# Kernel tuning notes

Measured on AMD Instinct MI355X. Metric: run time of the kernel, lower is better.

The kernel has to match this reference:

```python
import jax, jax.numpy as jnp
import numpy as np

N_USERS = 200000
N_ITEMS = 100000
EMBED_DIM = 64
N_LAYERS = 3
N_INTER = 1000000


def setup_inputs() -> dict:
    key = jax.random.key(0)
    k1, k2, k3, k4 = jax.random.split(key, 4)
    user_ids = jax.random.randint(k1, (N_INTER,), 0, N_USERS, dtype=jnp.int64 if jax.config.jax_enable_x64 else jnp.int32)
    item_ids = jax.random.randint(k2, (N_INTER,), 0, N_ITEMS, dtype=jnp.int64 if jax.config.jax_enable_x64 else jnp.int32)
    user_emb = jax.random.normal(k3, (N_USERS, EMBED_DIM), dtype=jnp.float32) * 0.1
    item_emb = jax.random.normal(k4, (N_ITEMS, EMBED_DIM), dtype=jnp.float32) * 0.1
    return {"user_emb": user_emb, "item_emb": item_emb, "user_ids": user_ids, "item_ids": item_ids}


def reference(user_emb, item_emb, user_ids, item_ids):
    n_users = user_emb.shape[0]
    n_items = item_emb.shape[0]
    n_nodes = n_users + n_items

    # Symmetric bipartite adjacency as directed edge list (both directions).
    src = jnp.concatenate([user_ids, item_ids + n_users])   # [2E]
    dst = jnp.concatenate([item_ids + n_users, user_ids])   # [2E]

    # Symmetric normalization D^{-1/2} A D^{-1/2} (duplicate edges sum, matching scipy CSR).
    deg = jax.ops.segment_sum(jnp.ones_like(src, dtype=jnp.float32), src, num_segments=n_nodes)
    d_inv_sqrt = jnp.where(deg > 0, jax.lax.rsqrt(jnp.maximum(deg, 1.0)), 0.0)
    w = d_inv_sqrt[src] * d_inv_sqrt[dst]                    # [2E] edge weights

    emb = jnp.concatenate([user_emb, item_emb], axis=0)      # [n_nodes, d]
    acc = emb
    for _ in range(N_LAYERS):
        # SpMM: out[dst] += w * emb[src]
        emb = jax.ops.segment_sum(w[:, None] * emb[src], dst, num_segments=n_nodes)
        acc = acc + emb
    final = acc / (N_LAYERS + 1)                             # mean over stacked layers
    return final[:n_users], final[n_users:]
```

## Files before the change

### kernel.cpp

```cpp
#include <hip/hip_runtime.h>

#define N_USERS 200000
#define N_ITEMS 100000
#define N_NODES 300000
#define DIM 64
#define N_INTER 1000000
#define N_EDGES (2 * N_INTER)

#define BSHIFT 10
#define BNODES (1 << BSHIFT)
#define NBUCKET ((N_NODES + BNODES - 1) >> BSHIFT)
#define TILE 4096
#define NBLK_P ((N_INTER + TILE - 1) / TILE)

#define NPW 8
#define NWAVE ((N_NODES + NPW - 1) / NPW)
#define GATHER_THREADS (NWAVE * 64)

typedef unsigned short bf16_t;
typedef unsigned int u32;

static __device__ __forceinline__ bf16_t f2bf(float f) {
    union { float f; u32 u; } v; v.f = f;
    u32 r = v.u + 0x7FFFu + ((v.u >> 16) & 1u);
    return (bf16_t)(r >> 16);
}
static __device__ __forceinline__ float bf2f(bf16_t h) {
    union { u32 u; float f; } v; v.u = ((u32)h) << 16;
    return v.f;
}
static __device__ __forceinline__ float bflo(u32 v) {
    union { u32 u; float f; } x; x.u = v << 16; return x.f;
}
static __device__ __forceinline__ float bfhi(u32 v) {
    union { u32 u; float f; } x; x.u = v & 0xFFFF0000u; return x.f;
}
static __device__ __forceinline__ u32 pack_bf16(float lo, float hi) {
    u32 r;
    asm("v_cvt_pk_bf16_f32 %0, %1, %2" : "=v"(r) : "v"(lo), "v"(hi));
    return r;
}

__global__ void hist_kernel(const int* __restrict__ uid, const int* __restrict__ iid,
                            u32* __restrict__ bucket_count) {
    __shared__ u32 h[NBUCKET];
    int t = threadIdx.x;
    for (int i = t; i < NBUCKET; i += 256) h[i] = 0;
    __syncthreads();
    int base = blockIdx.x * TILE;
    int end = base + TILE; if (end > N_INTER) end = N_INTER;
    for (int k = base + t; k < end; k += 256) {
        int u = uid[k];
        int it = N_USERS + iid[k];
        atomicAdd(&h[it >> BSHIFT], 1u);
        atomicAdd(&h[u >> BSHIFT], 1u);
    }
    __syncthreads();
    for (int i = t; i < NBUCKET; i += 256)
        if (h[i]) atomicAdd(&bucket_count[i], h[i]);
}

__global__ void scan_kernel(const u32* __restrict__ bucket_count, u32* __restrict__ bstart,
                            u32* __restrict__ bucket_cursor, u32* __restrict__ rowptr) {
    __shared__ u32 buf[2][512];
    int t = threadIdx.x;
    u32 v0 = (t < NBUCKET) ? bucket_count[t] : 0u;
    buf[0][t] = v0;
    __syncthreads();
    int s = 0;
    for (int off = 1; off < 512; off <<= 1) {
        u32 v = buf[s][t];
        if (t >= off) v += buf[s][t - off];
        buf[1 - s][t] = v;
        __syncthreads();
        s = 1 - s;
    }
    if (t < NBUCKET) {
        u32 excl = buf[s][t] - v0;
        bstart[t] = excl;
        bucket_cursor[t] = excl;
    }
    if (t == 0) {
        bstart[NBUCKET] = N_EDGES;
        rowptr[N_NODES] = N_EDGES;
    }
}

__global__ void place_kernel(const int* __restrict__ uid, const int* __restrict__ iid,
                             u32* __restrict__ bucket_cursor, u32* __restrict__ bdata) {
    __shared__ u32 h[NBUCKET];
    __shared__ u32 basesh[NBUCKET];
    int t = threadIdx.x;
    for (int i = t; i < NBUCKET; i += 256) h[i] = 0;
    __syncthreads();
    int base = blockIdx.x * TILE;
    int end = base + TILE; if (end > N_INTER) end = N_INTER;
    for (int k = base + t; k < end; k += 256) {
        int u = uid[k];
        int it = N_USERS + iid[k];
        atomicAdd(&h[it >> BSHIFT], 1u);
        atomicAdd(&h[u >> BSHIFT], 1u);
    }
    __syncthreads();
    for (int i = t; i < NBUCKET; i += 256) {
        u32 c = h[i];
        basesh[i] = c ? atomicAdd(&bucket_cursor[i], c) : 0u;
        h[i] = 0;
    }
    __syncthreads();
    for (int k = base + t; k < end; k += 256) {
        int u = uid[k];
        int it = N_USERS + iid[k];
        {
            int b = it >> BSHIFT;
            u32 pos = basesh[b] + atomicAdd(&h[b], 1u);
            bdata[pos] = (((u32)(it & (BNODES - 1))) << 19) | (u32)u;
        }
        {
            int b = u >> BSHIFT;
            u32 pos = basesh[b] + atomicAdd(&h[b], 1u);
            bdata[pos] = (((u32)(u & (BNODES - 1))) << 19) | (u32)it;
        }
    }
}

__global__ void csr_kernel(const u32* __restrict__ bstart, const u32* __restrict__ bdata,
                           u32* __restrict__ rowptr, float* __restrict__ dinv,
                           int* __restrict__ col) {
    __shared__ u32 cnt[BNODES];
    __shared__ u32 sb[2][BNODES];
    __shared__ u32 cur[BNODES];
    int b = blockIdx.x;
    int t = threadIdx.x;
    int nbase = b << BSHIFT;
    u32 bs = bstart[b], be = bstart[b + 1];
    u32 m = be - bs;

    #pragma unroll
    for (int j = 0; j < 4; ++j) cnt[t + j * 256] = 0;
    __syncthreads();
    for (u32 e = t; e < m; e += 256) {
        u32 v = bdata[bs + e];
        atomicAdd(&cnt[v >> 19], 1u);
    }
    __syncthreads();
    #pragma unroll
    for (int j = 0; j < 4; ++j) sb[0][t + j * 256] = cnt[t + j * 256];
    __syncthreads();
    int s = 0;
    for (int off = 1; off < BNODES; off <<= 1) {
        #pragma unroll
        for (int j = 0; j < 4; ++j) {
            int idx = t + j * 256;
            u32 v = sb[s][idx];
            if (idx >= off) v += sb[s][idx - off];
            sb[1 - s][idx] = v;
        }
        __syncthreads();
        s = 1 - s;
    }
    #pragma unroll
    for (int j = 0; j < 4; ++j) {
        int idx = t + j * 256;
        int node = nbase + idx;
        u32 c = cnt[idx];
        u32 excl = sb[s][idx] - c;
        cur[idx] = excl;
        if (node < N_NODES) {
            rowptr[node] = bs + excl;
            dinv[node] = (c > 0) ? rsqrtf((float)c) : 0.0f;
        }
    }
    __syncthreads();
    for (u32 e = t; e < m; e += 256) {
        u32 v = bdata[bs + e];
        u32 ln = v >> 19;
        u32 pos = atomicAdd(&cur[ln], 1u);
        col[bs + pos] = (int)(v & 0x7FFFFu);
    }
}

__global__ void ecol_kernel(const int* __restrict__ col, const float* __restrict__ dinv,
                            int2* __restrict__ ecol) {
    int e = blockIdx.x * blockDim.x + threadIdx.x;
    if (e < N_EDGES) {
        int s = col[e];
        ecol[e] = make_int2(s, __float_as_int(dinv[s]));
    }
}

__global__ void init_kernel(const float4* __restrict__ ue, const float4* __restrict__ ie,
                            ushort4* __restrict__ cur) {
    int idx = blockIdx.x * blockDim.x + threadIdx.x;
    if (idx < N_NODES * 16) {
        float4 v = (idx < N_USERS * 16) ? ue[idx] : ie[idx - N_USERS * 16];
        ushort4 h;
        h.x = f2bf(v.x); h.y = f2bf(v.y); h.z = f2bf(v.z); h.w = f2bf(v.w);
        cur[idx] = h;
    }
}

__global__ void gather_kernel(const u32* __restrict__ rowptr, const int2* __restrict__ ecol,
                              const float* __restrict__ dinv,
                              const u32* __restrict__ cur, u32* __restrict__ nxt) {
    int wid = (blockIdx.x * blockDim.x + threadIdx.x) >> 6;
    int lane = threadIdx.x & 63;
    int n0 = __builtin_amdgcn_readfirstlane(wid * NPW);
    if (n0 >= N_NODES) return;
    u32 rp[NPW + 1];
    #pragma unroll
    for (int i = 0; i <= NPW; ++i) rp[i] = rowptr[n0 + i];
    bool hi = (lane >> 5) != 0;
    u32 c = (u32)(lane & 31);
    #pragma unroll
    for (int pr = 0; pr < NPW; pr += 2) {
        u32 rsA = rp[pr],     lA = rp[pr + 1] - rp[pr];
        u32 rsB = rp[pr + 1], lB = rp[pr + 2] - rp[pr + 1];
        u32 mx = lA > lB ? lA : lB;
        float a0 = 0.0f, a1 = 0.0f;
        for (u32 p = 0; p < mx; p += 4) {
            #pragma unroll
            for (int q = 0; q < 4; ++q) {
                u32 st = p + (u32)q;
                u32 iA = rsA + st; if (iA >= (u32)N_EDGES) iA = N_EDGES - 1u;
                u32 iB = rsB + st; if (iB >= (u32)N_EDGES) iB = N_EDGES - 1u;
                iA = __builtin_amdgcn_readfirstlane((int)iA);
                iB = __builtin_amdgcn_readfirstlane((int)iB);
                int2 eA = ecol[iA];
                int2 eB = ecol[iB];
                u32 wAu = (st < lA) ? (u32)eA.y : 0u;
                u32 wBu = (st < lB) ? (u32)eB.y : 0u;
                u32 srow = hi ? (u32)eB.x : (u32)eA.x;
                float wf = __uint_as_float(hi ? wBu : wAu);
                u32 v = cur[(srow << 5) + c];
                a0 += wf * bflo(v);
                a1 += wf * bfhi(v);
            }
        }
        float sc = hi ? dinv[n0 + pr + 1] : dinv[n0 + pr];
        u32 orow = (((u32)(n0 + pr) + (hi ? 1u : 0u)) << 5) + c;
        nxt[orow] = pack_bf16(sc * a0, sc * a1);
    }
}

__global__ void gather_final_kernel(const u32* __restrict__ rowptr, const int2* __restrict__ ecol,
                                    const float* __restrict__ dinv,
                                    const u32* __restrict__ b1, const u32* __restrict__ b2,
                                    const float* __restrict__ ue, const float* __restrict__ ie,
                                    float* __restrict__ out) {
    int wid = (blockIdx.x * blockDim.x + threadIdx.x) >> 6;
    int lane = threadIdx.x & 63;
    int n0 = __builtin_amdgcn_readfirstlane(wid * NPW);
    if (n0 >= N_NODES) return;
    u32 rp[NPW + 1];
    #pragma unroll
    for (int i = 0; i <= NPW; ++i) rp[i] = rowptr[n0 + i];
    bool hi = (lane >> 5) != 0;
    u32 c = (u32)(lane & 31);
    #pragma unroll
    for (int pr = 0; pr < NPW; pr += 2) {
        u32 rsA = rp[pr],     lA = rp[pr + 1] - rp[pr];
        u32 rsB = rp[pr + 1], lB = rp[pr + 2] - rp[pr + 1];
        u32 mx = lA > lB ? lA : lB;
        float a0 = 0.0f, a1 = 0.0f;
        for (u32 p = 0; p < mx; p += 4) {
            #pragma unroll
            for (int q = 0; q < 4; ++q) {
                u32 st = p + (u32)q;
                u32 iA = rsA + st; if (iA >= (u32)N_EDGES) iA = N_EDGES - 1u;
                u32 iB = rsB + st; if (iB >= (u32)N_EDGES) iB = N_EDGES - 1u;
                iA = __builtin_amdgcn_readfirstlane((int)iA);
                iB = __builtin_amdgcn_readfirstlane((int)iB);
                int2 eA = ecol[iA];
                int2 eB = ecol[iB];
                u32 wAu = (st < lA) ? (u32)eA.y : 0u;
                u32 wBu = (st < lB) ? (u32)eB.y : 0u;
                u32 srow = hi ? (u32)eB.x : (u32)eA.x;
                float wf = __uint_as_float(hi ? wBu : wAu);
                u32 v = b2[(srow << 5) + c];
                a0 += wf * bflo(v);
                a1 += wf * bfhi(v);
            }
        }
        int n = n0 + pr + (hi ? 1 : 0);
        float sc = hi ? dinv[n0 + pr + 1] : dinv[n0 + pr];
        u32 o32 = (((u32)n) << 5) + c;
        u32 v1 = b1[o32], v2 = b2[o32];
        float2 e0 = (n < N_USERS) ? ((const float2*)ue)[o32]
                                  : ((const float2*)ie)[o32 - (u32)N_USERS * 32u];
        float ox = (e0.x + bflo(v1) + bflo(v2) + sc * a0) * 0.25f;
        float oy = (e0.y + bfhi(v1) + bfhi(v2) + sc * a1) * 0.25f;
        ((float2*)out)[o32] = make_float2(ox, oy);
    }
}

extern "C" void kernel_launch(void* const* d_in, const int* in_sizes, int n_in,
                              void* d_out, int out_size, void* d_ws, size_t ws_size,
                              hipStream_t stream) {
    const float* ue = (const float*)d_in[0];
    const float* ie = (const float*)d_in[1];
    const int* uid = (const int*)d_in[2];
    const int* iid = (const int*)d_in[3];
    float* out = (float*)d_out;

    char* ws = (char*)d_ws;
    size_t off = 0;
    auto alloc = [&](size_t bytes) { char* p = ws + off; off = (off + bytes + 255) & ~(size_t)255; return p; };
    u32*    bucket_count  = (u32*)alloc((size_t)NBUCKET * 4);
    u32*    bstart        = (u32*)alloc((size_t)(NBUCKET + 1) * 4);
    u32*    bucket_cursor = (u32*)alloc((size_t)NBUCKET * 4);
    u32*    rowptr        = (u32*)alloc((size_t)(N_NODES + 1) * 4);
    float*  dinv          = (float*)alloc((size_t)N_NODES * 4);
    u32*    bdata         = (u32*)alloc((size_t)N_EDGES * 4);
    int*    col           = (int*)alloc((size_t)N_EDGES * 4);
    int2*   ecol          = (int2*)alloc((size_t)N_EDGES * 8);
    bf16_t* buf0          = (bf16_t*)alloc((size_t)N_NODES * DIM * 2);
    bf16_t* buf1          = (bf16_t*)alloc((size_t)N_NODES * DIM * 2);
    bf16_t* buf2          = (bf16_t*)alloc((size_t)N_NODES * DIM * 2);

    hipMemsetAsync(bucket_count, 0, (size_t)NBUCKET * 4, stream);
    hist_kernel<<<NBLK_P, 256, 0, stream>>>(uid, iid, bucket_count);
    scan_kernel<<<1, 512, 0, stream>>>(bucket_count, bstart, bucket_cursor, rowptr);
    place_kernel<<<NBLK_P, 256, 0, stream>>>(uid, iid, bucket_cursor, bdata);
    csr_kernel<<<NBUCKET, 256, 0, stream>>>(bstart, bdata, rowptr, dinv, col);
    ecol_kernel<<<(N_EDGES + 255) / 256, 256, 0, stream>>>(col, dinv, ecol);

    init_kernel<<<(N_NODES * 16 + 255) / 256, 256, 0, stream>>>(
        (const float4*)ue, (const float4*)ie, (ushort4*)buf0);

    gather_kernel<<<(GATHER_THREADS + 255) / 256, 256, 0, stream>>>(
        rowptr, ecol, dinv, (const u32*)buf0, (u32*)buf1);
    gather_kernel<<<(GATHER_THREADS + 255) / 256, 256, 0, stream>>>(
        rowptr, ecol, dinv, (const u32*)buf1, (u32*)buf2);
    gather_final_kernel<<<(GATHER_THREADS + 255) / 256, 256, 0, stream>>>(
        rowptr, ecol, dinv, (const u32*)buf1, (const u32*)buf2, ue, ie, out);
}
```

Before: 424.2 us.

## Store per-block bucket histograms and compute placement offsets with a per-bucket scan

The hist kernel now writes each tile's bucket histogram to a workspace array. A new base_kernel scans those histograms across blocks for each bucket to produce exact write offsets. This lets place_kernel skip recounting its tile and skip the global atomic cursor reservation. Bucket size and tile size are also halved, which doubles the number of csr_kernel blocks and shrinks its shared-memory scan. In exchange the pipeline gains an extra launch and a strided read/write of the per-block histogram matrix.

```diff
diff --git a/kernel.cpp b/kernel.cpp
--- a/kernel.cpp
+++ b/kernel.cpp
@@ -7,10 +7,10 @@
 #define N_INTER 1000000
 #define N_EDGES (2 * N_INTER)
 
-#define BSHIFT 10
+#define BSHIFT 9
 #define BNODES (1 << BSHIFT)
 #define NBUCKET ((N_NODES + BNODES - 1) >> BSHIFT)
-#define TILE 4096
+#define TILE 2048
 #define NBLK_P ((N_INTER + TILE - 1) / TILE)
 
 #define NPW 8
@@ -42,7 +42,7 @@
 }
 
 __global__ void hist_kernel(const int* __restrict__ uid, const int* __restrict__ iid,
-                            u32* __restrict__ bucket_count) {
+                            u32* __restrict__ bucket_count, u32* __restrict__ bhist) {
     __shared__ u32 h[NBUCKET];
     int t = threadIdx.x;
     for (int i = t; i < NBUCKET; i += 256) h[i] = 0;
@@ -56,15 +56,41 @@
         atomicAdd(&h[u >> BSHIFT], 1u);
     }
     __syncthreads();
-    for (int i = t; i < NBUCKET; i += 256)
-        if (h[i]) atomicAdd(&bucket_count[i], h[i]);
+    u32* bh = bhist + (size_t)blockIdx.x * NBUCKET;
+    for (int i = t; i < NBUCKET; i += 256) {
+        u32 c = h[i];
+        bh[i] = c;
+        if (c) atomicAdd(&bucket_count[i], c);
+    }
 }
 
 __global__ void scan_kernel(const u32* __restrict__ bucket_count, u32* __restrict__ bstart,
-                            u32* __restrict__ bucket_cursor, u32* __restrict__ rowptr) {
+                            u32* __restrict__ rowptr) {
+    __shared__ u32 buf[2][1024];
+    int t = threadIdx.x;
+    u32 v0 = (t < NBUCKET) ? bucket_count[t] : 0u;
+    buf[0][t] = v0;
+    __syncthreads();
+    int s = 0;
+    for (int off = 1; off < 1024; off <<= 1) {
+        u32 v = buf[s][t];
+        if (t >= off) v += buf[s][t - off];
+        buf[1 - s][t] = v;
+        __syncthreads();
+        s = 1 - s;
+    }
+    if (t < NBUCKET) bstart[t] = buf[s][t] - v0;
+    if (t == 0) {
+        bstart[NBUCKET] = N_EDGES;
+        rowptr[N_NODES] = N_EDGES;
+    }
+}
+
+__global__ void base_kernel(const u32* __restrict__ bstart, u32* __restrict__ bhist) {
     __shared__ u32 buf[2][512];
-    int t = threadIdx.x;
-    u32 v0 = (t < NBUCKET) ? bucket_count[t] : 0u;
+    int bkt = blockIdx.x;
+    int t = threadIdx.x;
+    u32 v0 = (t < NBLK_P) ? bhist[(size_t)t * NBUCKET + bkt] : 0u;
     buf[0][t] = v0;
     __syncthreads();
     int s = 0;
@@ -75,39 +101,23 @@
         __syncthreads();
         s = 1 - s;
     }
-    if (t < NBUCKET) {
-        u32 excl = buf[s][t] - v0;
-        bstart[t] = excl;
-        bucket_cursor[t] = excl;
-    }
-    if (t == 0) {
-        bstart[NBUCKET] = N_EDGES;
-        rowptr[N_NODES] = N_EDGES;
-    }
+    if (t < NBLK_P)
+        bhist[(size_t)t * NBUCKET + bkt] = bstart[bkt] + (buf[s][t] - v0);
 }
 
 __global__ void place_kernel(const int* __restrict__ uid, const int* __restrict__ iid,
-                             u32* __restrict__ bucket_cursor, u32* __restrict__ bdata) {
+                             const u32* __restrict__ bhist, u32* __restrict__ bdata) {
     __shared__ u32 h[NBUCKET];
     __shared__ u32 basesh[NBUCKET];
     int t = threadIdx.x;
-    for (int i = t; i < NBUCKET; i += 256) h[i] = 0;
+    const u32* bh = bhist + (size_t)blockIdx.x * NBUCKET;
+    for (int i = t; i < NBUCKET; i += 256) {
+        basesh[i] = bh[i];
+        h[i] = 0;
+    }
     __syncthreads();
     int base = blockIdx.x * TILE;
     int end = base + TILE; if (end > N_INTER) end = N_INTER;
-    for (int k = base + t; k < end; k += 256) {
-        int u = uid[k];
-        int it = N_USERS + iid[k];
-        atomicAdd(&h[it >> BSHIFT], 1u);
-        atomicAdd(&h[u >> BSHIFT], 1u);
-    }
-    __syncthreads();
-    for (int i = t; i < NBUCKET; i += 256) {
-        u32 c = h[i];
-        basesh[i] = c ? atomicAdd(&bucket_cursor[i], c) : 0u;
-        h[i] = 0;
-    }
-    __syncthreads();
     for (int k = base + t; k < end; k += 256) {
         int u = uid[k];
         int it = N_USERS + iid[k];
@@ -137,7 +147,7 @@
     u32 m = be - bs;
 
     #pragma unroll
-    for (int j = 0; j < 4; ++j) cnt[t + j * 256] = 0;
+    for (int j = 0; j < BNODES / 256; ++j) cnt[t + j * 256] = 0;
     __syncthreads();
     for (u32 e = t; e < m; e += 256) {
         u32 v = bdata[bs + e];
@@ -145,12 +155,12 @@
     }
     __syncthreads();
     #pragma unroll
-    for (int j = 0; j < 4; ++j) sb[0][t + j * 256] = cnt[t + j * 256];
+    for (int j = 0; j < BNODES / 256; ++j) sb[0][t + j * 256] = cnt[t + j * 256];
     __syncthreads();
     int s = 0;
     for (int off = 1; off < BNODES; off <<= 1) {
         #pragma unroll
-        for (int j = 0; j < 4; ++j) {
+        for (int j = 0; j < BNODES / 256; ++j) {
             int idx = t + j * 256;
             u32 v = sb[s][idx];
             if (idx >= off) v += sb[s][idx - off];
@@ -160,7 +170,7 @@
         s = 1 - s;
     }
     #pragma unroll
-    for (int j = 0; j < 4; ++j) {
+    for (int j = 0; j < BNODES / 256; ++j) {
         int idx = t + j * 256;
         int node = nbase + idx;
         u32 c = cnt[idx];
@@ -308,7 +318,7 @@
     auto alloc = [&](size_t bytes) { char* p = ws + off; off = (off + bytes + 255) & ~(size_t)255; return p; };
     u32*    bucket_count  = (u32*)alloc((size_t)NBUCKET * 4);
     u32*    bstart        = (u32*)alloc((size_t)(NBUCKET + 1) * 4);
-    u32*    bucket_cursor = (u32*)alloc((size_t)NBUCKET * 4);
+    u32*    bhist         = (u32*)alloc((size_t)NBLK_P * NBUCKET * 4);
     u32*    rowptr        = (u32*)alloc((size_t)(N_NODES + 1) * 4);
     float*  dinv          = (float*)alloc((size_t)N_NODES * 4);
     u32*    bdata         = (u32*)alloc((size_t)N_EDGES * 4);
@@ -319,9 +329,10 @@
     bf16_t* buf2          = (bf16_t*)alloc((size_t)N_NODES * DIM * 2);
 
     hipMemsetAsync(bucket_count, 0, (size_t)NBUCKET * 4, stream);
-    hist_kernel<<<NBLK_P, 256, 0, stream>>>(uid, iid, bucket_count);
-    scan_kernel<<<1, 512, 0, stream>>>(bucket_count, bstart, bucket_cursor, rowptr);
-    place_kernel<<<NBLK_P, 256, 0, stream>>>(uid, iid, bucket_cursor, bdata);
+    hist_kernel<<<NBLK_P, 256, 0, stream>>>(uid, iid, bucket_count, bhist);
+    scan_kernel<<<1, 1024, 0, stream>>>(bucket_count, bstart, rowptr);
+    base_kernel<<<NBUCKET, 512, 0, stream>>>(bstart, bhist);
+    place_kernel<<<NBLK_P, 256, 0, stream>>>(uid, iid, bhist, bdata);
     csr_kernel<<<NBUCKET, 256, 0, stream>>>(bstart, bdata, rowptr, dinv, col);
     ecol_kernel<<<(N_EDGES + 255) / 256, 256, 0, stream>>>(col, dinv, ecol);
 
```

Result: no change. 423.7 us (-0.1%).

## Build CSR via global per-node degree atomics and direct edge placement

Applied to the files above, without the earlier changes.

Replaces the bucketed two-level CSR build (bucket histogram, bucket placement, per-bucket local sort, separate ecol pass) with a per-node global atomic degree count, a three-stage block scan for rowptr, and a place kernel that writes (neighbor, dinv) pairs straight into ecol using per-node atomic cursors. This removes the intermediate bdata and col arrays and two passes over the edges. In exchange it relies on global atomics scattered across 300K nodes, and edge order within a row becomes nondeterministic, which can change the bf16 accumulation order and makes gather reads of neighbors less ordered.

```diff
diff --git a/kernel.cpp b/kernel.cpp
--- a/kernel.cpp
+++ b/kernel.cpp
@@ -7,11 +7,8 @@
 #define N_INTER 1000000
 #define N_EDGES (2 * N_INTER)
 
-#define BSHIFT 10
-#define BNODES (1 << BSHIFT)
-#define NBUCKET ((N_NODES + BNODES - 1) >> BSHIFT)
-#define TILE 4096
-#define NBLK_P ((N_INTER + TILE - 1) / TILE)
+#define SBLK 1024
+#define NSB ((N_NODES + SBLK - 1) / SBLK)
 
 #define NPW 8
 #define NWAVE ((N_NODES + NPW - 1) / NPW)
@@ -25,10 +22,6 @@
     u32 r = v.u + 0x7FFFu + ((v.u >> 16) & 1u);
     return (bf16_t)(r >> 16);
 }
-static __device__ __forceinline__ float bf2f(bf16_t h) {
-    union { u32 u; float f; } v; v.u = ((u32)h) << 16;
-    return v.f;
-}
 static __device__ __forceinline__ float bflo(u32 v) {
     union { u32 u; float f; } x; x.u = v << 16; return x.f;
 }
@@ -41,30 +34,41 @@
     return r;
 }
 
-__global__ void hist_kernel(const int* __restrict__ uid, const int* __restrict__ iid,
-                            u32* __restrict__ bucket_count) {
-    __shared__ u32 h[NBUCKET];
-    int t = threadIdx.x;
-    for (int i = t; i < NBUCKET; i += 256) h[i] = 0;
-    __syncthreads();
-    int base = blockIdx.x * TILE;
-    int end = base + TILE; if (end > N_INTER) end = N_INTER;
-    for (int k = base + t; k < end; k += 256) {
+__global__ void deg_kernel(const int* __restrict__ uid, const int* __restrict__ iid,
+                           u32* __restrict__ deg) {
+    int k = blockIdx.x * blockDim.x + threadIdx.x;
+    if (k < N_INTER) {
         int u = uid[k];
         int it = N_USERS + iid[k];
-        atomicAdd(&h[it >> BSHIFT], 1u);
-        atomicAdd(&h[u >> BSHIFT], 1u);
-    }
+        atomicAdd(&deg[it], 1u);
+        atomicAdd(&deg[u], 1u);
+    }
+}
+
+__global__ void s1_kernel(const u32* __restrict__ deg, u32* __restrict__ bsum) {
+    __shared__ u32 red[256];
+    int b = blockIdx.x, t = threadIdx.x;
+    int base = b * SBLK;
+    u32 s = 0;
+    #pragma unroll
+    for (int j = 0; j < 4; ++j) {
+        int idx = base + t + j * 256;
+        if (idx < N_NODES) s += deg[idx];
+    }
+    red[t] = s;
     __syncthreads();
-    for (int i = t; i < NBUCKET; i += 256)
-        if (h[i]) atomicAdd(&bucket_count[i], h[i]);
-}
-
-__global__ void scan_kernel(const u32* __restrict__ bucket_count, u32* __restrict__ bstart,
-                            u32* __restrict__ bucket_cursor, u32* __restrict__ rowptr) {
+    for (int off = 128; off > 0; off >>= 1) {
+        if (t < off) red[t] += red[t + off];
+        __syncthreads();
+    }
+    if (t == 0) bsum[b] = red[0];
+}
+
+__global__ void s2_kernel(const u32* __restrict__ bsum, u32* __restrict__ bbase,
+                          u32* __restrict__ rowptr) {
     __shared__ u32 buf[2][512];
     int t = threadIdx.x;
-    u32 v0 = (t < NBUCKET) ? bucket_count[t] : 0u;
+    u32 v0 = (t < NSB) ? bsum[t] : 0u;
     buf[0][t] = v0;
     __syncthreads();
     int s = 0;
@@ -75,117 +79,64 @@
         __syncthreads();
         s = 1 - s;
     }
-    if (t < NBUCKET) {
-        u32 excl = buf[s][t] - v0;
-        bstart[t] = excl;
-        bucket_cursor[t] = excl;
-    }
-    if (t == 0) {
-        bstart[NBUCKET] = N_EDGES;
-        rowptr[N_NODES] = N_EDGES;
-    }
-}
-
-__global__ void place_kernel(const int* __restrict__ uid, const int* __restrict__ iid,
-                             u32* __restrict__ bucket_cursor, u32* __restrict__ bdata) {
-    __shared__ u32 h[NBUCKET];
-    __shared__ u32 basesh[NBUCKET];
-    int t = threadIdx.x;
-    for (int i = t; i < NBUCKET; i += 256) h[i] = 0;
-    __syncthreads();
-    int base = blockIdx.x * TILE;
-    int end = base + TILE; if (end > N_INTER) end = N_INTER;
-    for (int k = base + t; k < end; k += 256) {
-        int u = uid[k];
-        int it = N_USERS + iid[k];
-        atomicAdd(&h[it >> BSHIFT], 1u);
-        atomicAdd(&h[u >> BSHIFT], 1u);
-    }
-    __syncthreads();
-    for (int i = t; i < NBUCKET; i += 256) {
-        u32 c = h[i];
-        basesh[i] = c ? atomicAdd(&bucket_cursor[i], c) : 0u;
-        h[i] = 0;
-    }
-    __syncthreads();
-    for (int k = base + t; k < end; k += 256) {
-        int u = uid[k];
-        int it = N_USERS + iid[k];
-        {
-            int b = it >> BSHIFT;
-            u32 pos = basesh[b] + atomicAdd(&h[b], 1u);
-            bdata[pos] = (((u32)(it & (BNODES - 1))) << 19) | (u32)u;
-        }
-        {
-            int b = u >> BSHIFT;
-            u32 pos = basesh[b] + atomicAdd(&h[b], 1u);
-            bdata[pos] = (((u32)(u & (BNODES - 1))) << 19) | (u32)it;
-        }
-    }
-}
-
-__global__ void csr_kernel(const u32* __restrict__ bstart, const u32* __restrict__ bdata,
-                           u32* __restrict__ rowptr, float* __restrict__ dinv,
-                           int* __restrict__ col) {
-    __shared__ u32 cnt[BNODES];
-    __shared__ u32 sb[2][BNODES];
-    __shared__ u32 cur[BNODES];
-    int b = blockIdx.x;
-    int t = threadIdx.x;
-    int nbase = b << BSHIFT;
-    u32 bs = bstart[b], be = bstart[b + 1];
-    u32 m = be - bs;
-
-    #pragma unroll
-    for (int j = 0; j < 4; ++j) cnt[t + j * 256] = 0;
-    __syncthreads();
-    for (u32 e = t; e < m; e += 256) {
-        u32 v = bdata[bs + e];
-        atomicAdd(&cnt[v >> 19], 1u);
-    }
-    __syncthreads();
-    #pragma unroll
-    for (int j = 0; j < 4; ++j) sb[0][t + j * 256] = cnt[t + j * 256];
+    if (t < NSB) bbase[t] = buf[s][t] - v0;
+    if (t == 0) rowptr[N_NODES] = N_EDGES;
+}
+
+__global__ void s3_kernel(const u32* __restrict__ deg, const u32* __restrict__ bbase,
+                          u32* __restrict__ rowptr, u32* __restrict__ gcur,
+                          float* __restrict__ dinv) {
+    __shared__ u32 sb[2][SBLK];
+    int b = blockIdx.x, t = threadIdx.x;
+    int base = b * SBLK;
+    u32 v[4];
+    #pragma unroll
+    for (int j = 0; j < 4; ++j) {
+        int idx = t + j * 256;
+        int node = base + idx;
+        v[j] = (node < N_NODES) ? deg[node] : 0u;
+        sb[0][idx] = v[j];
+    }
     __syncthreads();
     int s = 0;
-    for (int off = 1; off < BNODES; off <<= 1) {
+    for (int off = 1; off < SBLK; off <<= 1) {
         #pragma unroll
         for (int j = 0; j < 4; ++j) {
             int idx = t + j * 256;
-            u32 v = sb[s][idx];
-            if (idx >= off) v += sb[s][idx - off];
-            sb[1 - s][idx] = v;
+            u32 x = sb[s][idx];
+            if (idx >= off) x += sb[s][idx - off];
+            sb[1 - s][idx] = x;
         }
         __syncthreads();
         s = 1 - s;
     }
+    u32 bb = bbase[b];
     #pragma unroll
     for (int j = 0; j < 4; ++j) {
         int idx = t + j * 256;
-        int node = nbase + idx;
-        u32 c = cnt[idx];
-        u32 excl = sb[s][idx] - c;
-        cur[idx] = excl;
+        int node = base + idx;
         if (node < N_NODES) {
-            rowptr[node] = bs + excl;
-            dinv[node] = (c > 0) ? rsqrtf((float)c) : 0.0f;
-        }
-    }
-    __syncthreads();
-    for (u32 e = t; e < m; e += 256) {
-        u32 v = bdata[bs + e];
-        u32 ln = v >> 19;
-        u32 pos = atomicAdd(&cur[ln], 1u);
-        col[bs + pos] = (int)(v & 0x7FFFFu);
-    }
-}
-
-__global__ void ecol_kernel(const int* __restrict__ col, const float* __restrict__ dinv,
-                            int2* __restrict__ ecol) {
-    int e = blockIdx.x * blockDim.x + threadIdx.x;
-    if (e < N_EDGES) {
-        int s = col[e];
-        ecol[e] = make_int2(s, __float_as_int(dinv[s]));
+            u32 rp = bb + (sb[s][idx] - v[j]);
+            rowptr[node] = rp;
+            gcur[node] = rp;
+            dinv[node] = v[j] ? rsqrtf((float)v[j]) : 0.0f;
+        }
+    }
+}
+
+__global__ void place_kernel(const int* __restrict__ uid, const int* __restrict__ iid,
+                             const float* __restrict__ dinv, u32* __restrict__ gcur,
+                             int2* __restrict__ ecol) {
+    int k = blockIdx.x * blockDim.x + threadIdx.x;
+    if (k < N_INTER) {
+        int u = uid[k];
+        int it = N_USERS + iid[k];
+        float du = dinv[u];
+        float di = dinv[it];
+        u32 p1 = atomicAdd(&gcur[it], 1u);
+        ecol[p1] = make_int2(u, __float_as_int(du));
+        u32 p2 = atomicAdd(&gcur[u], 1u);
+        ecol[p2] = make_int2(it, __float_as_int(di));
     }
 }
 
@@ -306,24 +257,23 @@
     char* ws = (char*)d_ws;
     size_t off = 0;
     auto alloc = [&](size_t bytes) { char* p = ws + off; off = (off + bytes + 255) & ~(size_t)255; return p; };
-    u32*    bucket_count  = (u32*)alloc((size_t)NBUCKET * 4);
-    u32*    bstart        = (u32*)alloc((size_t)(NBUCKET + 1) * 4);
-    u32*    bucket_cursor = (u32*)alloc((size_t)NBUCKET * 4);
-    u32*    rowptr        = (u32*)alloc((size_t)(N_NODES + 1) * 4);
-    float*  dinv          = (float*)alloc((size_t)N_NODES * 4);
-    u32*    bdata         = (u32*)alloc((size_t)N_EDGES * 4);
-    int*    col           = (int*)alloc((size_t)N_EDGES * 4);
-    int2*   ecol          = (int2*)alloc((size_t)N_EDGES * 8);
-    bf16_t* buf0          = (bf16_t*)alloc((size_t)N_NODES * DIM * 2);
-    bf16_t* buf1          = (bf16_t*)alloc((size_t)N_NODES * DIM * 2);
-    bf16_t* buf2          = (bf16_t*)alloc((size_t)N_NODES * DIM * 2);
-
-    hipMemsetAsync(bucket_count, 0, (size_t)NBUCKET * 4, stream);
-    hist_kernel<<<NBLK_P, 256, 0, stream>>>(uid, iid, bucket_count);
-    scan_kernel<<<1, 512, 0, stream>>>(bucket_count, bstart, bucket_cursor, rowptr);
-    place_kernel<<<NBLK_P, 256, 0, stream>>>(uid, iid, bucket_cursor, bdata);
-    csr_kernel<<<NBUCKET, 256, 0, stream>>>(bstart, bdata, rowptr, dinv, col);
-    ecol_kernel<<<(N_EDGES + 255) / 256, 256, 0, stream>>>(col, dinv, ecol);
+    u32*    deg     = (u32*)alloc((size_t)N_NODES * 4);
+    u32*    bsum    = (u32*)alloc((size_t)NSB * 4);
+    u32*    bbase   = (u32*)alloc((size_t)NSB * 4);
+    u32*    rowptr  = (u32*)alloc((size_t)(N_NODES + 1) * 4);
+    u32*    gcur    = (u32*)alloc((size_t)N_NODES * 4);
+    float*  dinv    = (float*)alloc((size_t)N_NODES * 4);
+    int2*   ecol    = (int2*)alloc((size_t)N_EDGES * 8);
+    bf16_t* buf0    = (bf16_t*)alloc((size_t)N_NODES * DIM * 2);
+    bf16_t* buf1    = (bf16_t*)alloc((size_t)N_NODES * DIM * 2);
+    bf16_t* buf2    = (bf16_t*)alloc((size_t)N_NODES * DIM * 2);
+
+    hipMemsetAsync(deg, 0, (size_t)N_NODES * 4, stream);
+    deg_kernel<<<(N_INTER + 255) / 256, 256, 0, stream>>>(uid, iid, deg);
+    s1_kernel<<<NSB, 256, 0, stream>>>(deg, bsum);
+    s2_kernel<<<1, 512, 0, stream>>>(bsum, bbase, rowptr);
+    s3_kernel<<<NSB, 256, 0, stream>>>(deg, bbase, rowptr, gcur, dinv);
+    place_kernel<<<(N_INTER + 255) / 256, 256, 0, stream>>>(uid, iid, dinv, gcur, ecol);
 
     init_kernel<<<(N_NODES * 16 + 255) / 256, 256, 0, stream>>>(
         (const float4*)ue, (const float4*)ie, (ushort4*)buf0);
```

Result: slower. 550.5 us (+29.8%).
